# Kernel optimization log

Hardware: AMD Instinct MI355X
Metric: run time of the kernel (lower is better)

The kernel has to match this reference:

```python
import jax, jax.numpy as jnp
import numpy as np
from jax import lax


def setup_inputs() -> dict:
    key = jax.random.key(0)
    inputs = jax.random.normal(key, (8, 512, 512, 2), dtype=jnp.float32)
    return {"inputs": inputs, "filter_size": 21}


def reference(inputs, filter_size):
    B, H, W, C = inputs.shape
    fs = int(filter_size)
    kval = 1.0 / float(fs * fs)  # flat dilation2d kernel value
    num_passes = max(H, W) // (fs // 2)

    scoremap_softmax = jax.nn.softmax(inputs, axis=-1)
    scoremap_foreground = jnp.max(scoremap_softmax[..., 1:], axis=-1)  # [B,H,W]
    detmap_foreground = jnp.round(scoremap_foreground)                 # [B,H,W] binary

    # find_max_location: (row, col) of the per-image max of the foreground map
    flat_idx = jnp.argmax(scoremap_foreground.reshape(B, -1), axis=-1)
    rows = flat_idx // W
    cols = flat_idx % W

    def grow(det_i, r, c):
        # sparse seed: single 1.0 at the max location
        seed = jnp.zeros((H, W), dtype=jnp.float32).at[r, c].set(1.0)

        def step(objectmap, _):
            # tf.nn.dilation2d with a flat kernel of value kval == max-pool + kval.
            # All values are >= 0, so init value 0.0 matches -inf padding semantics.
            dil = lax.reduce_window(objectmap, 0.0, lax.max,
                                    (fs, fs), (1, 1), 'SAME') + kval
            return jnp.round(det_i * dil), None

        out, _ = lax.scan(step, seed, None, length=num_passes)
        return out

    maps = jax.vmap(grow)(detmap_foreground, rows, cols)  # [B,H,W]
    maps = maps[..., None]                                # [B,H,W,1]
    # Faithful to the (buggy) nested python loops: B copies of the B maps stacked.
    return jnp.tile(maps, (B, 1, 1, 1))                   # [B*B,H,W,1]
```

## Files before the change

kernel.cpp:

```cpp
#include <hip/hip_runtime.h>
#include <stdint.h>

#define HH 512
#define WW 512
#define NB 8
#define RAD 10
#define NPASS 51
#define WPR 16
#define IMG_WORDS (HH*WPR)
#define STRIDE 540
#define GLO 12
#define RPT 16

__global__ __launch_bounds__(256) void k_det(const float* __restrict__ in,
                                             uint32_t* __restrict__ det,
                                             unsigned long long* __restrict__ keys) {
    __shared__ unsigned long long red[4];
    int tid  = blockIdx.x * 256 + threadIdx.x;
    int lane = threadIdx.x & 63;
    int wv   = threadIdx.x >> 6;
    int wave = tid >> 6;
    long long base = (long long)wave * 256;
    unsigned long long best = 0;
    const float2* in2 = (const float2*)in;
    #pragma unroll
    for (int j = 0; j < 4; ++j) {
        long long p = base + j * 64 + lane;
        float2 v = in2[p];
        float d = v.y - v.x;
        int pred = (d > 0.0f);
        unsigned long long bits = __ballot(pred);
        if (lane == 0) ((unsigned long long*)det)[wave * 4 + j] = bits;
        uint32_t du = __float_as_uint(d);
        uint32_t mono = (du & 0x80000000u) ? ~du : (du | 0x80000000u);
        uint32_t pix = (uint32_t)(p & (HH * WW - 1));
        unsigned long long key = ((unsigned long long)mono << 32)
                               | (unsigned long long)(0xFFFFFFFFu - pix);
        best = key > best ? key : best;
    }
    #pragma unroll
    for (int s = 32; s > 0; s >>= 1) {
        unsigned long long o = __shfl_xor(best, s);
        best = o > best ? o : best;
    }
    if (lane == 0) red[wv] = best;
    __syncthreads();
    if (threadIdx.x == 0) {
        unsigned long long b0 = red[0], b1 = red[1], b2 = red[2], b3 = red[3];
        b0 = b0 > b1 ? b0 : b1;
        b2 = b2 > b3 ? b2 : b3;
        keys[blockIdx.x] = b0 > b2 ? b0 : b2;
    }
}

__global__ __launch_bounds__(512) void k_grow(const uint32_t* __restrict__ det,
                                              const unsigned long long* __restrict__ keys,
                                              uint32_t* __restrict__ outmask) {
    __shared__ __align__(16) uint32_t hb[2][WPR * STRIDE];
    __shared__ uint32_t flag[NPASS];
    __shared__ unsigned long long redk[4];
    int b    = blockIdx.x;
    int t    = threadIdx.x;
    int lane = t & 63;
    int wvid = t >> 6;
    int w    = t & 15;
    int r0   = (t >> 4) << 4;
    uint32_t dreg[RPT];
    const uint32_t* db = det + b * IMG_WORDS;
    #pragma unroll
    for (int k = 0; k < RPT; ++k) dreg[k] = db[(r0 + k) * WPR + w];

    unsigned long long kk = (t < 256) ? keys[b * 256 + t] : 0ull;
    #pragma unroll
    for (int s = 32; s > 0; s >>= 1) {
        unsigned long long o = __shfl_xor(kk, s);
        kk = o > kk ? o : kk;
    }
    if (lane == 0 && wvid < 4) redk[wvid] = kk;

    for (int i = t; i < 2 * WPR * STRIDE; i += 512) ((uint32_t*)hb)[i] = 0;
    if (t < NPASS) flag[t] = 0;
    __syncthreads();

    unsigned long long key = redk[0];
    key = redk[1] > key ? redk[1] : key;
    key = redk[2] > key ? redk[2] : key;
    key = redk[3] > key ? redk[3] : key;
    uint32_t pix = 0xFFFFFFFFu - (uint32_t)key;
    int sr = pix >> 9, sc = pix & 511;
    uint32_t curreg[RPT];
    #pragma unroll
    for (int k = 0; k < RPT; ++k)
        curreg[k] = (sr == r0 + k && (sc >> 5) == w) ? (1u << (sc & 31)) : 0u;

    for (int it = 0; it < NPASS; ++it) {
        uint32_t* colv = &hb[it & 1][w * STRIDE];
        uint32_t Dv[RPT];
        #pragma unroll
        for (int k = 0; k < RPT; ++k) {
            uint32_t bb = curreg[k];
            uint32_t a = (uint32_t)__builtin_amdgcn_update_dpp(
                0, (int)bb, 0x111, 0xF, 0xF, true);
            uint32_t c = (uint32_t)__builtin_amdgcn_update_dpp(
                0, (int)bb, 0x101, 0xF, 0xF, true);
            unsigned long long W = (unsigned long long)(a >> 22)
                                 | ((unsigned long long)bb << 10)
                                 | ((unsigned long long)c << 42);
            unsigned long long D = W | (W >> 1);
            D |= D >> 2;
            D |= D >> 4;
            unsigned long long D7 = D;
            D |= D >> 8;
            D |= D7 >> 13;
            Dv[k] = (uint32_t)D;
        }
        *(uint4*)&colv[r0 + GLO]      = make_uint4(Dv[0],  Dv[1],  Dv[2],  Dv[3]);
        *(uint4*)&colv[r0 + GLO + 4]  = make_uint4(Dv[4],  Dv[5],  Dv[6],  Dv[7]);
        *(uint4*)&colv[r0 + GLO + 8]  = make_uint4(Dv[8],  Dv[9],  Dv[10], Dv[11]);
        *(uint4*)&colv[r0 + GLO + 12] = make_uint4(Dv[12], Dv[13], Dv[14], Dv[15]);
        __syncthreads();

        if (it > 0 && flag[it - 1] == 0) break;

        uint32_t x[36];
        {
            uint2 a0 = *(const uint2*)&colv[r0 + 2];
            uint4 a1 = *(const uint4*)&colv[r0 + 4];
            uint4 a2 = *(const uint4*)&colv[r0 + 8];
            uint4 b0 = *(const uint4*)&colv[r0 + 28];
            uint4 b1 = *(const uint4*)&colv[r0 + 32];
            uint2 b2 = *(const uint2*)&colv[r0 + 36];
            x[0] = a0.x;  x[1] = a0.y;
            x[2] = a1.x;  x[3] = a1.y;  x[4] = a1.z;  x[5] = a1.w;
            x[6] = a2.x;  x[7] = a2.y;  x[8] = a2.z;  x[9] = a2.w;
            #pragma unroll
            for (int k = 0; k < RPT; ++k) x[10 + k] = Dv[k];
            x[26] = b0.x; x[27] = b0.y; x[28] = b0.z; x[29] = b0.w;
            x[30] = b1.x; x[31] = b1.y; x[32] = b1.z; x[33] = b1.w;
            x[34] = b2.x; x[35] = b2.y;
        }
        uint32_t s[21];
        s[20] = x[20];
        #pragma unroll
        for (int i = 19; i >= 0; --i) s[i] = x[i] | s[i + 1];
        uint32_t p[36];
        p[21] = x[21];
        #pragma unroll
        for (int i = 22; i < 36; ++i) p[i] = x[i] | p[i - 1];
        uint32_t diff = 0;
        {
            uint32_t nv = dreg[0] & s[0];
            diff |= nv ^ curreg[0];
            curreg[0] = nv;
        }
        #pragma unroll
        for (int k = 1; k < RPT; ++k) {
            uint32_t nv = dreg[k] & (s[k] | p[k + 20]);
            diff |= nv ^ curreg[k];
            curreg[k] = nv;
        }
        if (diff) flag[it] = 1;
    }
    #pragma unroll
    for (int k = 0; k < RPT; ++k)
        outmask[b * IMG_WORDS + (r0 + k) * WPR + w] = curreg[k];
}

__global__ __launch_bounds__(256) void k_expand(const uint32_t* __restrict__ mask,
                                                float* __restrict__ out) {
    int t   = blockIdx.x * 256 + threadIdx.x;
    int img = t >> 16;
    int pix = (t & 65535) << 2;
    uint32_t wv = mask[(img & 7) * IMG_WORDS + (pix >> 5)];
    int sh = pix & 31;
    float4 o;
    o.x = (wv >> (sh + 0)) & 1 ? 1.0f : 0.0f;
    o.y = (wv >> (sh + 1)) & 1 ? 1.0f : 0.0f;
    o.z = (wv >> (sh + 2)) & 1 ? 1.0f : 0.0f;
    o.w = (wv >> (sh + 3)) & 1 ? 1.0f : 0.0f;
    ((float4*)out)[t] = o;
}

extern "C" void kernel_launch(void* const* d_in, const int* in_sizes, int n_in,
                              void* d_out, int out_size, void* d_ws, size_t ws_size,
                              hipStream_t stream) {
    const float* in = (const float*)d_in[0];
    float* out = (float*)d_out;
    unsigned long long* keys = (unsigned long long*)d_ws;
    uint32_t* det = (uint32_t*)((char*)d_ws + 2048 * 8);
    uint32_t* fin = (uint32_t*)((char*)d_ws + 2048 * 8 + NB * IMG_WORDS * 4);

    k_det   <<<2048,  256, 0, stream>>>(in, det, keys);
    k_grow  <<<NB,    512, 0, stream>>>(det, keys, fin);
    k_expand<<<16384, 256, 0, stream>>>(fin, out);
}
```

Measured before the change: 106.4 us.

## Split region growing across row segments with halo exchange via global flags

The grow kernel moves from one block per image to eight blocks per image. Each block owns 64 rows plus a 32-row halo and runs 3 dilation passes locally, then exchanges boundary rows with its neighbour blocks through global memory and spin-wait release/acquire flags. This spreads the serial 51-pass recurrence across more CUs and shrinks shared memory per block. In exchange it drops the early-exit convergence check, always runs 51 passes, adds inter-block synchronisation that assumes all 64 blocks are co-resident, and needs an extra memset launch.

```diff
diff --git a/kernel.cpp b/kernel.cpp
--- a/kernel.cpp
+++ b/kernel.cpp
@@ -3,14 +3,25 @@
 
 #define HH 512
 #define WW 512
-#define NB 8
+#define NIMG 8
+#define SEGS 8
+#define OWNR 64
+#define HALO 32
 #define RAD 10
-#define NPASS 51
+#define KPP 3
+#define NPER 17
 #define WPR 16
 #define IMG_WORDS (HH*WPR)
-#define STRIDE 540
+#define CSTR 156
 #define GLO 12
-#define RPT 16
+#define RPT 8
+
+__device__ inline void gstore(uint32_t* p, uint32_t v) {
+    __hip_atomic_store(p, v, __ATOMIC_RELAXED, __HIP_MEMORY_SCOPE_AGENT);
+}
+__device__ inline uint32_t gload(const uint32_t* p) {
+    return __hip_atomic_load(p, __ATOMIC_RELAXED, __HIP_MEMORY_SCOPE_AGENT);
+}
 
 __global__ __launch_bounds__(256) void k_det(const float* __restrict__ in,
                                              uint32_t* __restrict__ det,
@@ -53,33 +64,41 @@
     }
 }
 
-__global__ __launch_bounds__(512) void k_grow(const uint32_t* __restrict__ det,
+__global__ __launch_bounds__(256) void k_grow(const uint32_t* __restrict__ det,
                                               const unsigned long long* __restrict__ keys,
-                                              uint32_t* __restrict__ outmask) {
-    __shared__ __align__(16) uint32_t hb[2][WPR * STRIDE];
-    __shared__ uint32_t flag[NPASS];
+                                              uint32_t* __restrict__ fin,
+                                              uint32_t* __restrict__ gobj,
+                                              uint32_t* __restrict__ flags) {
+    __shared__ __align__(16) uint32_t hb[2][WPR * CSTR];
     __shared__ unsigned long long redk[4];
-    int b    = blockIdx.x;
+    int blk  = blockIdx.x;
+    int img  = blk & 7;
+    int seg  = blk >> 3;
     int t    = threadIdx.x;
     int lane = t & 63;
     int wvid = t >> 6;
     int w    = t & 15;
-    int r0   = (t >> 4) << 4;
+    int g    = t >> 4;
+    int R0   = seg * OWNR;
+    int gr0  = R0 - HALO + g * RPT;
+
     uint32_t dreg[RPT];
-    const uint32_t* db = det + b * IMG_WORDS;
-    #pragma unroll
-    for (int k = 0; k < RPT; ++k) dreg[k] = db[(r0 + k) * WPR + w];
-
-    unsigned long long kk = (t < 256) ? keys[b * 256 + t] : 0ull;
+    const uint32_t* db = det + img * IMG_WORDS;
+    #pragma unroll
+    for (int k = 0; k < RPT; ++k) {
+        int r = gr0 + k;
+        dreg[k] = (r >= 0 && r < HH) ? db[r * WPR + w] : 0u;
+    }
+
+    unsigned long long kk = keys[img * 256 + t];
     #pragma unroll
     for (int s = 32; s > 0; s >>= 1) {
         unsigned long long o = __shfl_xor(kk, s);
         kk = o > kk ? o : kk;
     }
-    if (lane == 0 && wvid < 4) redk[wvid] = kk;
-
-    for (int i = t; i < 2 * WPR * STRIDE; i += 512) ((uint32_t*)hb)[i] = 0;
-    if (t < NPASS) flag[t] = 0;
+    if (lane == 0) redk[wvid] = kk;
+
+    for (int i = t; i < 2 * WPR * CSTR; i += 256) ((uint32_t*)hb)[i] = 0;
     __syncthreads();
 
     unsigned long long key = redk[0];
@@ -91,79 +110,113 @@
     uint32_t curreg[RPT];
     #pragma unroll
     for (int k = 0; k < RPT; ++k)
-        curreg[k] = (sr == r0 + k && (sc >> 5) == w) ? (1u << (sc & 31)) : 0u;
-
-    for (int it = 0; it < NPASS; ++it) {
-        uint32_t* colv = &hb[it & 1][w * STRIDE];
-        uint32_t Dv[RPT];
+        curreg[k] = (gr0 + k == sr && (sc >> 5) == w) ? (1u << (sc & 31)) : 0u;
+
+    int it = 0;
+    for (int per = 0; per < NPER; ++per) {
         #pragma unroll
-        for (int k = 0; k < RPT; ++k) {
-            uint32_t bb = curreg[k];
-            uint32_t a = (uint32_t)__builtin_amdgcn_update_dpp(
-                0, (int)bb, 0x111, 0xF, 0xF, true);
-            uint32_t c = (uint32_t)__builtin_amdgcn_update_dpp(
-                0, (int)bb, 0x101, 0xF, 0xF, true);
-            unsigned long long W = (unsigned long long)(a >> 22)
-                                 | ((unsigned long long)bb << 10)
-                                 | ((unsigned long long)c << 42);
-            unsigned long long D = W | (W >> 1);
-            D |= D >> 2;
-            D |= D >> 4;
-            unsigned long long D7 = D;
-            D |= D >> 8;
-            D |= D7 >> 13;
-            Dv[k] = (uint32_t)D;
-        }
-        *(uint4*)&colv[r0 + GLO]      = make_uint4(Dv[0],  Dv[1],  Dv[2],  Dv[3]);
-        *(uint4*)&colv[r0 + GLO + 4]  = make_uint4(Dv[4],  Dv[5],  Dv[6],  Dv[7]);
-        *(uint4*)&colv[r0 + GLO + 8]  = make_uint4(Dv[8],  Dv[9],  Dv[10], Dv[11]);
-        *(uint4*)&colv[r0 + GLO + 12] = make_uint4(Dv[12], Dv[13], Dv[14], Dv[15]);
+        for (int j = 0; j < KPP; ++j, ++it) {
+            uint32_t* colv = &hb[it & 1][w * CSTR];
+            uint32_t Dv[RPT];
+            #pragma unroll
+            for (int k = 0; k < RPT; ++k) {
+                uint32_t bb = curreg[k];
+                uint32_t a = (uint32_t)__builtin_amdgcn_update_dpp(
+                    0, (int)bb, 0x111, 0xF, 0xF, true);
+                uint32_t c = (uint32_t)__builtin_amdgcn_update_dpp(
+                    0, (int)bb, 0x101, 0xF, 0xF, true);
+                unsigned long long W = (unsigned long long)(a >> 22)
+                                     | ((unsigned long long)bb << 10)
+                                     | ((unsigned long long)c << 42);
+                unsigned long long D = W | (W >> 1);
+                D |= D >> 2;
+                D |= D >> 4;
+                unsigned long long D7 = D;
+                D |= D >> 8;
+                D |= D7 >> 13;
+                Dv[k] = (uint32_t)D;
+            }
+            int r0 = g * RPT;
+            *(uint4*)&colv[r0 + GLO]     = make_uint4(Dv[0], Dv[1], Dv[2], Dv[3]);
+            *(uint4*)&colv[r0 + GLO + 4] = make_uint4(Dv[4], Dv[5], Dv[6], Dv[7]);
+            __syncthreads();
+
+            uint32_t x[28];
+            {
+                uint2 a0 = *(const uint2*)&colv[r0 + 2];
+                uint4 a1 = *(const uint4*)&colv[r0 + 4];
+                uint4 a2 = *(const uint4*)&colv[r0 + 8];
+                uint4 b0 = *(const uint4*)&colv[r0 + 20];
+                uint4 b1 = *(const uint4*)&colv[r0 + 24];
+                uint2 b2 = *(const uint2*)&colv[r0 + 28];
+                x[0] = a0.x;  x[1] = a0.y;
+                x[2] = a1.x;  x[3] = a1.y;  x[4] = a1.z;  x[5] = a1.w;
+                x[6] = a2.x;  x[7] = a2.y;  x[8] = a2.z;  x[9] = a2.w;
+                #pragma unroll
+                for (int k = 0; k < RPT; ++k) x[10 + k] = Dv[k];
+                x[18] = b0.x; x[19] = b0.y; x[20] = b0.z; x[21] = b0.w;
+                x[22] = b1.x; x[23] = b1.y; x[24] = b1.z; x[25] = b1.w;
+                x[26] = b2.x; x[27] = b2.y;
+            }
+            uint32_t s[21];
+            s[20] = x[20];
+            #pragma unroll
+            for (int i = 19; i >= 0; --i) s[i] = x[i] | s[i + 1];
+            uint32_t p[28];
+            p[21] = x[21];
+            #pragma unroll
+            for (int i = 22; i < 28; ++i) p[i] = x[i] | p[i - 1];
+            curreg[0] = dreg[0] & s[0];
+            #pragma unroll
+            for (int k = 1; k < RPT; ++k)
+                curreg[k] = dreg[k] & (s[k] | p[k + 20]);
+        }
+        if (per == NPER - 1) break;
+
+        uint32_t* gb = gobj + ((per & 1) * NIMG + img) * IMG_WORDS;
+        if (g >= 4 && g < 12) {
+            #pragma unroll
+            for (int k = 0; k < RPT; ++k)
+                gstore(&gb[(gr0 + k) * WPR + w], curreg[k]);
+        }
+        __threadfence();
         __syncthreads();
-
-        if (it > 0 && flag[it - 1] == 0) break;
-
-        uint32_t x[36];
-        {
-            uint2 a0 = *(const uint2*)&colv[r0 + 2];
-            uint4 a1 = *(const uint4*)&colv[r0 + 4];
-            uint4 a2 = *(const uint4*)&colv[r0 + 8];
-            uint4 b0 = *(const uint4*)&colv[r0 + 28];
-            uint4 b1 = *(const uint4*)&colv[r0 + 32];
-            uint2 b2 = *(const uint2*)&colv[r0 + 36];
-            x[0] = a0.x;  x[1] = a0.y;
-            x[2] = a1.x;  x[3] = a1.y;  x[4] = a1.z;  x[5] = a1.w;
-            x[6] = a2.x;  x[7] = a2.y;  x[8] = a2.z;  x[9] = a2.w;
-            #pragma unroll
-            for (int k = 0; k < RPT; ++k) x[10 + k] = Dv[k];
-            x[26] = b0.x; x[27] = b0.y; x[28] = b0.z; x[29] = b0.w;
-            x[30] = b1.x; x[31] = b1.y; x[32] = b1.z; x[33] = b1.w;
-            x[34] = b2.x; x[35] = b2.y;
-        }
-        uint32_t s[21];
-        s[20] = x[20];
+        uint32_t* fl = &flags[img * 8];
+        if (t == 0)
+            __hip_atomic_store(&fl[seg], (uint32_t)(per + 1),
+                               __ATOMIC_RELEASE, __HIP_MEMORY_SCOPE_AGENT);
+        if (t == 0 && seg > 0) {
+            for (int z = 0; z < (1 << 24); ++z) {
+                if (__hip_atomic_load(&fl[seg - 1], __ATOMIC_ACQUIRE,
+                                      __HIP_MEMORY_SCOPE_AGENT) > (uint32_t)per) break;
+                __builtin_amdgcn_s_sleep(1);
+            }
+        }
+        if (t == 1 && seg < SEGS - 1) {
+            for (int z = 0; z < (1 << 24); ++z) {
+                if (__hip_atomic_load(&fl[seg + 1], __ATOMIC_ACQUIRE,
+                                      __HIP_MEMORY_SCOPE_AGENT) > (uint32_t)per) break;
+                __builtin_amdgcn_s_sleep(1);
+            }
+        }
+        __syncthreads();
+        if (g < 4 && seg > 0) {
+            #pragma unroll
+            for (int k = 0; k < RPT; ++k)
+                curreg[k] = gload(&gb[(gr0 + k) * WPR + w]);
+        }
+        if (g >= 12 && seg < SEGS - 1) {
+            #pragma unroll
+            for (int k = 0; k < RPT; ++k)
+                curreg[k] = gload(&gb[(gr0 + k) * WPR + w]);
+        }
+        __syncthreads();
+    }
+    if (g >= 4 && g < 12) {
         #pragma unroll
-        for (int i = 19; i >= 0; --i) s[i] = x[i] | s[i + 1];
-        uint32_t p[36];
-        p[21] = x[21];
-        #pragma unroll
-        for (int i = 22; i < 36; ++i) p[i] = x[i] | p[i - 1];
-        uint32_t diff = 0;
-        {
-            uint32_t nv = dreg[0] & s[0];
-            diff |= nv ^ curreg[0];
-            curreg[0] = nv;
-        }
-        #pragma unroll
-        for (int k = 1; k < RPT; ++k) {
-            uint32_t nv = dreg[k] & (s[k] | p[k + 20]);
-            diff |= nv ^ curreg[k];
-            curreg[k] = nv;
-        }
-        if (diff) flag[it] = 1;
-    }
-    #pragma unroll
-    for (int k = 0; k < RPT; ++k)
-        outmask[b * IMG_WORDS + (r0 + k) * WPR + w] = curreg[k];
+        for (int k = 0; k < RPT; ++k)
+            fin[img * IMG_WORDS + (gr0 + k) * WPR + w] = curreg[k];
+    }
 }
 
 __global__ __launch_bounds__(256) void k_expand(const uint32_t* __restrict__ mask,
@@ -186,11 +239,14 @@
                               hipStream_t stream) {
     const float* in = (const float*)d_in[0];
     float* out = (float*)d_out;
-    unsigned long long* keys = (unsigned long long*)d_ws;
-    uint32_t* det = (uint32_t*)((char*)d_ws + 2048 * 8);
-    uint32_t* fin = (uint32_t*)((char*)d_ws + 2048 * 8 + NB * IMG_WORDS * 4);
-
-    k_det   <<<2048,  256, 0, stream>>>(in, det, keys);
-    k_grow  <<<NB,    512, 0, stream>>>(det, keys, fin);
-    k_expand<<<16384, 256, 0, stream>>>(fin, out);
-}
+    uint32_t* flags            = (uint32_t*)d_ws;
+    unsigned long long* keys   = (unsigned long long*)((char*)d_ws + 4096);
+    uint32_t* det              = (uint32_t*)((char*)d_ws + 20480);
+    uint32_t* fin              = (uint32_t*)((char*)d_ws + 282624);
+    uint32_t* gobj             = (uint32_t*)((char*)d_ws + 544768);
+
+    hipMemsetAsync(flags, 0, 256, stream);
+    k_det   <<<2048,        256, 0, stream>>>(in, det, keys);
+    k_grow  <<<NIMG * SEGS, 256, 0, stream>>>(det, keys, fin, gobj, flags);
+    k_expand<<<16384,       256, 0, stream>>>(fin, out);
+}
```

Result: slower. 156.4 us (+47.0%).

## Skip dilation work for row groups whose neighbourhood did not change

Applied to the files above, without the earlier changes.

Replaces the single global per-pass change flag with per-wave, per-16-row-group change bitmasks in a rotating triple buffer. A wave only recomputes its horizontal dilation and vertical OR when its own or adjacent row groups changed in the previous pass, so stable regions are skipped. It rewrites cached shared-memory columns into the alternate buffer once after it stops computing. The added ballot and bitmask bookkeeping costs some overhead, and the wave-uniform skip condition only saves time when whole waves become inactive.

```diff
diff --git a/kernel.cpp b/kernel.cpp
--- a/kernel.cpp
+++ b/kernel.cpp
@@ -57,7 +57,7 @@
                                               const unsigned long long* __restrict__ keys,
                                               uint32_t* __restrict__ outmask) {
     __shared__ __align__(16) uint32_t hb[2][WPR * STRIDE];
-    __shared__ uint32_t flag[NPASS];
+    __shared__ unsigned long long chg[3];
     __shared__ unsigned long long redk[4];
     int b    = blockIdx.x;
     int t    = threadIdx.x;
@@ -79,7 +79,7 @@
     if (lane == 0 && wvid < 4) redk[wvid] = kk;
 
     for (int i = t; i < 2 * WPR * STRIDE; i += 512) ((uint32_t*)hb)[i] = 0;
-    if (t < NPASS) flag[t] = 0;
+    if (t == 0) { chg[0] = 0; chg[1] = 0; chg[2] = 0; }
     __syncthreads();
 
     unsigned long long key = redk[0];
@@ -93,73 +93,102 @@
     for (int k = 0; k < RPT; ++k)
         curreg[k] = (sr == r0 + k && (sc >> 5) == w) ? (1u << (sc & 31)) : 0u;
 
+    unsigned long long wm = 0xFull << (8 * wvid);
+    if (wvid > 0) wm |= 0xCull << (8 * (wvid - 1));
+    if (wvid < 7) wm |= 0x3ull << (8 * (wvid + 1));
+
+    uint32_t Dv[RPT];
+    bool bufs_ok = true;
+    int a = 0, z = 1, e = 2;
+
     for (int it = 0; it < NPASS; ++it) {
+        unsigned long long sk = chg[z];
+        bool comp = (it < 2) || ((sk & wm) != 0ull);
         uint32_t* colv = &hb[it & 1][w * STRIDE];
-        uint32_t Dv[RPT];
-        #pragma unroll
-        for (int k = 0; k < RPT; ++k) {
-            uint32_t bb = curreg[k];
-            uint32_t a = (uint32_t)__builtin_amdgcn_update_dpp(
-                0, (int)bb, 0x111, 0xF, 0xF, true);
-            uint32_t c = (uint32_t)__builtin_amdgcn_update_dpp(
-                0, (int)bb, 0x101, 0xF, 0xF, true);
-            unsigned long long W = (unsigned long long)(a >> 22)
-                                 | ((unsigned long long)bb << 10)
-                                 | ((unsigned long long)c << 42);
-            unsigned long long D = W | (W >> 1);
-            D |= D >> 2;
-            D |= D >> 4;
-            unsigned long long D7 = D;
-            D |= D >> 8;
-            D |= D7 >> 13;
-            Dv[k] = (uint32_t)D;
+        if (comp) {
+            #pragma unroll
+            for (int k = 0; k < RPT; ++k) {
+                uint32_t bb = curreg[k];
+                uint32_t aa = (uint32_t)__builtin_amdgcn_update_dpp(
+                    0, (int)bb, 0x111, 0xF, 0xF, true);
+                uint32_t cc = (uint32_t)__builtin_amdgcn_update_dpp(
+                    0, (int)bb, 0x101, 0xF, 0xF, true);
+                unsigned long long W = (unsigned long long)(aa >> 22)
+                                     | ((unsigned long long)bb << 10)
+                                     | ((unsigned long long)cc << 42);
+                unsigned long long D = W | (W >> 1);
+                D |= D >> 2;
+                D |= D >> 4;
+                unsigned long long D7 = D;
+                D |= D >> 8;
+                D |= D7 >> 13;
+                Dv[k] = (uint32_t)D;
+            }
+            bufs_ok = false;
+            *(uint4*)&colv[r0 + GLO]      = make_uint4(Dv[0],  Dv[1],  Dv[2],  Dv[3]);
+            *(uint4*)&colv[r0 + GLO + 4]  = make_uint4(Dv[4],  Dv[5],  Dv[6],  Dv[7]);
+            *(uint4*)&colv[r0 + GLO + 8]  = make_uint4(Dv[8],  Dv[9],  Dv[10], Dv[11]);
+            *(uint4*)&colv[r0 + GLO + 12] = make_uint4(Dv[12], Dv[13], Dv[14], Dv[15]);
+        } else if (!bufs_ok) {
+            *(uint4*)&colv[r0 + GLO]      = make_uint4(Dv[0],  Dv[1],  Dv[2],  Dv[3]);
+            *(uint4*)&colv[r0 + GLO + 4]  = make_uint4(Dv[4],  Dv[5],  Dv[6],  Dv[7]);
+            *(uint4*)&colv[r0 + GLO + 8]  = make_uint4(Dv[8],  Dv[9],  Dv[10], Dv[11]);
+            *(uint4*)&colv[r0 + GLO + 12] = make_uint4(Dv[12], Dv[13], Dv[14], Dv[15]);
+            bufs_ok = true;
         }
-        *(uint4*)&colv[r0 + GLO]      = make_uint4(Dv[0],  Dv[1],  Dv[2],  Dv[3]);
-        *(uint4*)&colv[r0 + GLO + 4]  = make_uint4(Dv[4],  Dv[5],  Dv[6],  Dv[7]);
-        *(uint4*)&colv[r0 + GLO + 8]  = make_uint4(Dv[8],  Dv[9],  Dv[10], Dv[11]);
-        *(uint4*)&colv[r0 + GLO + 12] = make_uint4(Dv[12], Dv[13], Dv[14], Dv[15]);
         __syncthreads();
 
-        if (it > 0 && flag[it - 1] == 0) break;
-
-        uint32_t x[36];
-        {
-            uint2 a0 = *(const uint2*)&colv[r0 + 2];
-            uint4 a1 = *(const uint4*)&colv[r0 + 4];
-            uint4 a2 = *(const uint4*)&colv[r0 + 8];
-            uint4 b0 = *(const uint4*)&colv[r0 + 28];
-            uint4 b1 = *(const uint4*)&colv[r0 + 32];
-            uint2 b2 = *(const uint2*)&colv[r0 + 36];
-            x[0] = a0.x;  x[1] = a0.y;
-            x[2] = a1.x;  x[3] = a1.y;  x[4] = a1.z;  x[5] = a1.w;
-            x[6] = a2.x;  x[7] = a2.y;  x[8] = a2.z;  x[9] = a2.w;
-            #pragma unroll
-            for (int k = 0; k < RPT; ++k) x[10 + k] = Dv[k];
-            x[26] = b0.x; x[27] = b0.y; x[28] = b0.z; x[29] = b0.w;
-            x[30] = b1.x; x[31] = b1.y; x[32] = b1.z; x[33] = b1.w;
-            x[34] = b2.x; x[35] = b2.y;
+        if (it >= 1 && chg[e] == 0ull) break;
+        if (t == 0) chg[z] = 0;
+
+        if (comp) {
+            uint32_t x[36];
+            {
+                uint2 a0 = *(const uint2*)&colv[r0 + 2];
+                uint4 a1 = *(const uint4*)&colv[r0 + 4];
+                uint4 a2 = *(const uint4*)&colv[r0 + 8];
+                uint4 b0 = *(const uint4*)&colv[r0 + 28];
+                uint4 b1 = *(const uint4*)&colv[r0 + 32];
+                uint2 b2 = *(const uint2*)&colv[r0 + 36];
+                x[0] = a0.x;  x[1] = a0.y;
+                x[2] = a1.x;  x[3] = a1.y;  x[4] = a1.z;  x[5] = a1.w;
+                x[6] = a2.x;  x[7] = a2.y;  x[8] = a2.z;  x[9] = a2.w;
+                #pragma unroll
+                for (int k = 0; k < RPT; ++k) x[10 + k] = Dv[k];
+                x[26] = b0.x; x[27] = b0.y; x[28] = b0.z; x[29] = b0.w;
+                x[30] = b1.x; x[31] = b1.y; x[32] = b1.z; x[33] = b1.w;
+                x[34] = b2.x; x[35] = b2.y;
+            }
+            uint32_t s[21];
+            s[20] = x[20];
+            #pragma unroll
+            for (int i = 19; i >= 0; --i) s[i] = x[i] | s[i + 1];
+            uint32_t p[36];
+            p[21] = x[21];
+            #pragma unroll
+            for (int i = 22; i < 36; ++i) p[i] = x[i] | p[i - 1];
+            uint32_t diff = 0;
+            {
+                uint32_t nv = dreg[0] & s[0];
+                diff |= nv ^ curreg[0];
+                curreg[0] = nv;
+            }
+            #pragma unroll
+            for (int k = 1; k < RPT; ++k) {
+                uint32_t nv = dreg[k] & (s[k] | p[k + 20]);
+                diff |= nv ^ curreg[k];
+                curreg[k] = nv;
+            }
+            unsigned long long bl = __ballot(diff != 0);
+            if (lane == 0) {
+                uint32_t nib = (((bl & 0xFFFFull)        != 0) ? 1u : 0u)
+                             | ((((bl >> 16) & 0xFFFFull) != 0) ? 2u : 0u)
+                             | ((((bl >> 32) & 0xFFFFull) != 0) ? 4u : 0u)
+                             | (((bl >> 48)               != 0) ? 8u : 0u);
+                ((uint8_t*)chg)[a * 8 + wvid] = (uint8_t)nib;
+            }
         }
-        uint32_t s[21];
-        s[20] = x[20];
-        #pragma unroll
-        for (int i = 19; i >= 0; --i) s[i] = x[i] | s[i + 1];
-        uint32_t p[36];
-        p[21] = x[21];
-        #pragma unroll
-        for (int i = 22; i < 36; ++i) p[i] = x[i] | p[i - 1];
-        uint32_t diff = 0;
-        {
-            uint32_t nv = dreg[0] & s[0];
-            diff |= nv ^ curreg[0];
-            curreg[0] = nv;
-        }
-        #pragma unroll
-        for (int k = 1; k < RPT; ++k) {
-            uint32_t nv = dreg[k] & (s[k] | p[k + 20]);
-            diff |= nv ^ curreg[k];
-            curreg[k] = nv;
-        }
-        if (diff) flag[it] = 1;
+        int tmp = a; a = z; z = e; e = tmp;
     }
     #pragma unroll
     for (int k = 0; k < RPT; ++k)
```

Measured after the change: 105.6 us. Within noise of the previous version (-0.8%).

## Replace block barrier with neighbor-wave flag sync and use doubling OR window

Applied to the files above, without the earlier changes.

The per-pass __syncthreads in the region-grow loop is replaced by point-to-point sync. Each wave publishes its iteration counter in LDS and spin-waits only on the two adjacent waves whose rows it reads from the halo. The global convergence flag and early break are removed, so every image always runs all passes. The vertical 21-row OR is now computed with a log-doubling tree instead of prefix/suffix scans. This cuts barrier stalls and scan work, at the cost of spin-wait loops with an arbitrary timeout and losing early termination when growth converges sooner.

```diff
diff --git a/kernel.cpp b/kernel.cpp
--- a/kernel.cpp
+++ b/kernel.cpp
@@ -57,7 +57,7 @@
                                               const unsigned long long* __restrict__ keys,
                                               uint32_t* __restrict__ outmask) {
     __shared__ __align__(16) uint32_t hb[2][WPR * STRIDE];
-    __shared__ uint32_t flag[NPASS];
+    __shared__ uint32_t ep[8];
     __shared__ unsigned long long redk[4];
     int b    = blockIdx.x;
     int t    = threadIdx.x;
@@ -79,7 +79,7 @@
     if (lane == 0 && wvid < 4) redk[wvid] = kk;
 
     for (int i = t; i < 2 * WPR * STRIDE; i += 512) ((uint32_t*)hb)[i] = 0;
-    if (t < NPASS) flag[t] = 0;
+    if (t < 8) ep[t] = 0;
     __syncthreads();
 
     unsigned long long key = redk[0];
@@ -99,13 +99,13 @@
         #pragma unroll
         for (int k = 0; k < RPT; ++k) {
             uint32_t bb = curreg[k];
-            uint32_t a = (uint32_t)__builtin_amdgcn_update_dpp(
+            uint32_t aa = (uint32_t)__builtin_amdgcn_update_dpp(
                 0, (int)bb, 0x111, 0xF, 0xF, true);
-            uint32_t c = (uint32_t)__builtin_amdgcn_update_dpp(
+            uint32_t cc = (uint32_t)__builtin_amdgcn_update_dpp(
                 0, (int)bb, 0x101, 0xF, 0xF, true);
-            unsigned long long W = (unsigned long long)(a >> 22)
+            unsigned long long W = (unsigned long long)(aa >> 22)
                                  | ((unsigned long long)bb << 10)
-                                 | ((unsigned long long)c << 42);
+                                 | ((unsigned long long)cc << 42);
             unsigned long long D = W | (W >> 1);
             D |= D >> 2;
             D |= D >> 4;
@@ -118,9 +118,23 @@
         *(uint4*)&colv[r0 + GLO + 4]  = make_uint4(Dv[4],  Dv[5],  Dv[6],  Dv[7]);
         *(uint4*)&colv[r0 + GLO + 8]  = make_uint4(Dv[8],  Dv[9],  Dv[10], Dv[11]);
         *(uint4*)&colv[r0 + GLO + 12] = make_uint4(Dv[12], Dv[13], Dv[14], Dv[15]);
-        __syncthreads();
-
-        if (it > 0 && flag[it - 1] == 0) break;
+
+        if (lane == 0)
+            __hip_atomic_store(&ep[wvid], (uint32_t)(it + 1),
+                               __ATOMIC_RELEASE, __HIP_MEMORY_SCOPE_WORKGROUP);
+        uint32_t tgt = (uint32_t)(it + 1);
+        if (wvid > 0) {
+            int z = 0;
+            while (__hip_atomic_load(&ep[wvid - 1], __ATOMIC_ACQUIRE,
+                                     __HIP_MEMORY_SCOPE_WORKGROUP) < tgt
+                   && z < (1 << 24)) { ++z; }
+        }
+        if (wvid < 7) {
+            int z = 0;
+            while (__hip_atomic_load(&ep[wvid + 1], __ATOMIC_ACQUIRE,
+                                     __HIP_MEMORY_SCOPE_WORKGROUP) < tgt
+                   && z < (1 << 24)) { ++z; }
+        }
 
         uint32_t x[36];
         {
@@ -139,27 +153,21 @@
             x[30] = b1.x; x[31] = b1.y; x[32] = b1.z; x[33] = b1.w;
             x[34] = b2.x; x[35] = b2.y;
         }
-        uint32_t s[21];
-        s[20] = x[20];
-        #pragma unroll
-        for (int i = 19; i >= 0; --i) s[i] = x[i] | s[i + 1];
-        uint32_t p[36];
-        p[21] = x[21];
-        #pragma unroll
-        for (int i = 22; i < 36; ++i) p[i] = x[i] | p[i - 1];
-        uint32_t diff = 0;
-        {
-            uint32_t nv = dreg[0] & s[0];
-            diff |= nv ^ curreg[0];
-            curreg[0] = nv;
-        }
-        #pragma unroll
-        for (int k = 1; k < RPT; ++k) {
-            uint32_t nv = dreg[k] & (s[k] | p[k + 20]);
-            diff |= nv ^ curreg[k];
-            curreg[k] = nv;
-        }
-        if (diff) flag[it] = 1;
+        uint32_t w1[35];
+        #pragma unroll
+        for (int i = 0; i < 35; ++i) w1[i] = x[i] | x[i + 1];
+        uint32_t w2[33];
+        #pragma unroll
+        for (int i = 0; i < 33; ++i) w2[i] = w1[i] | w1[i + 2];
+        uint32_t w4[29];
+        #pragma unroll
+        for (int i = 0; i < 29; ++i) w4[i] = w2[i] | w2[i + 4];
+        uint32_t w8[21];
+        #pragma unroll
+        for (int i = 0; i < 21; ++i) w8[i] = w4[i] | w4[i + 8];
+        #pragma unroll
+        for (int k = 0; k < RPT; ++k)
+            curreg[k] = dreg[k] & (w8[k] | w8[k + 5]);
     }
     #pragma unroll
     for (int k = 0; k < RPT; ++k)
```

Measured after the change: 120.5 us. +13.2%, slower.
